# Optimization experiments

Hardware: AMD Instinct MI355X
Metric: run time of the kernel (lower is better)

Reference implementation:

```python
import jax, jax.numpy as jnp
import numpy as np

N, T, S, E, H, DFF = 4, 2048, 2048, 512, 8, 2048
DH = E // H
EPS = 1e-5


def layer_norm(x, w, b):
    m = jnp.mean(x, axis=-1, keepdims=True)
    v = jnp.mean(jnp.square(x - m), axis=-1, keepdims=True)
    return (x - m) * jax.lax.rsqrt(v + EPS) * w + b


def mha(q, k, v, wq, bq, wk, bk, wv, bv, wo, bo, mask=None):
    # q: (N,Tq,E), k/v: (N,Tk,E); torch Linear convention: y = x @ W.T + b
    Nq, Tq, _ = q.shape
    Tk = k.shape[1]
    Q = (q @ wq.T + bq).reshape(Nq, Tq, H, DH).transpose(0, 2, 1, 3)  # (N,H,Tq,DH)
    K = (k @ wk.T + bk).reshape(Nq, Tk, H, DH).transpose(0, 2, 1, 3)
    V = (v @ wv.T + bv).reshape(Nq, Tk, H, DH).transpose(0, 2, 1, 3)
    scores = jnp.einsum('bhtd,bhsd->bhts', Q, K) * (1.0 / np.sqrt(DH))  # (N,H,Tq,Tk)
    if mask is not None:
        scores = jnp.where(mask, scores, jnp.float32(-1e9))
    attn = jax.nn.softmax(scores, axis=-1)
    out = jnp.einsum('bhts,bhsd->bhtd', attn, V)  # (N,H,Tq,DH)
    out = out.transpose(0, 2, 1, 3).reshape(Nq, Tq, E)
    return out @ wo.T + bo


def setup_inputs() -> dict:
    key = jax.random.key(0)
    ks = jax.random.split(key, 20)
    s = 0.02

    def lin(k, out_d, in_d):
        return jax.random.normal(k, (out_d, in_d), jnp.float32) * s

    inp = {
        'tgt': jax.random.normal(ks[0], (N, T, E), jnp.float32),
        'memory': jax.random.normal(ks[1], (N, S, E), jnp.float32),
        'tgt_mask': jnp.tril(jnp.ones((T, T), dtype=bool)),  # causal (T,T)
        # self-attention params
        'sa_wq': lin(ks[2], E, E), 'sa_bq': jnp.zeros((E,), jnp.float32),
        'sa_wk': lin(ks[3], E, E), 'sa_bk': jnp.zeros((E,), jnp.float32),
        'sa_wv': lin(ks[4], E, E), 'sa_bv': jnp.zeros((E,), jnp.float32),
        'sa_wo': lin(ks[5], E, E), 'sa_bo': jnp.zeros((E,), jnp.float32),
        # cross-attention params
        'ca_wq': lin(ks[6], E, E), 'ca_bq': jnp.zeros((E,), jnp.float32),
        'ca_wk': lin(ks[7], E, E), 'ca_bk': jnp.zeros((E,), jnp.float32),
        'ca_wv': lin(ks[8], E, E), 'ca_bv': jnp.zeros((E,), jnp.float32),
        'ca_wo': lin(ks[9], E, E), 'ca_bo': jnp.zeros((E,), jnp.float32),
        # FFN params
        'w1': lin(ks[10], DFF, E), 'b1': jnp.zeros((DFF,), jnp.float32),
        'w2': lin(ks[11], E, DFF), 'b2': jnp.zeros((E,), jnp.float32),
        # LayerNorm params
        'ln1_w': jnp.ones((E,), jnp.float32), 'ln1_b': jnp.zeros((E,), jnp.float32),
        'ln2_w': jnp.ones((E,), jnp.float32), 'ln2_b': jnp.zeros((E,), jnp.float32),
        'ln3_w': jnp.ones((E,), jnp.float32), 'ln3_b': jnp.zeros((E,), jnp.float32),
    }
    return inp


def reference(tgt, memory, tgt_mask,
              sa_wq, sa_bq, sa_wk, sa_bk, sa_wv, sa_bv, sa_wo, sa_bo,
              ca_wq, ca_bq, ca_wk, ca_bk, ca_wv, ca_bv, ca_wo, ca_bo,
              w1, b1, w2, b2,
              ln1_w, ln1_b, ln2_w, ln2_b, ln3_w, ln3_b):
    # stage 1: masked self-attention + residual + LN (dropout=0 / eval mode)
    sa = mha(tgt, tgt, tgt, sa_wq, sa_bq, sa_wk, sa_bk, sa_wv, sa_bv, sa_wo, sa_bo, mask=tgt_mask)
    x = layer_norm(tgt + sa, ln1_w, ln1_b)
    # stage 2: cross-attention over encoder memory + residual + LN
    ca = mha(x, memory, memory, ca_wq, ca_bq, ca_wk, ca_bk, ca_wv, ca_bv, ca_wo, ca_bo)
    x = layer_norm(x + ca, ln2_w, ln2_b)
    # stage 3: FFN (ReLU) + residual + LN
    mlp = jax.nn.relu(x @ w1.T + b1) @ w2.T + b2
    out = layer_norm(x + mlp, ln3_w, ln3_b)
    return out
```

## Files before the change

### kernel.cpp

```cpp
#include <hip/hip_runtime.h>
#include <hip/hip_bf16.h>
#include <cstdint>

typedef short short8 __attribute__((ext_vector_type(8)));
typedef short short4v __attribute__((ext_vector_type(4)));
typedef float f32x4 __attribute__((ext_vector_type(4)));
typedef float f32x16 __attribute__((ext_vector_type(16)));

#define GLL16(gp, lp) __builtin_amdgcn_global_load_lds( \
    (const __attribute__((address_space(1))) unsigned int*)(gp), \
    (__attribute__((address_space(3))) unsigned int*)(lp), 16, 0, 0)

__device__ __forceinline__ float bf2f(ushort u) {
    union { unsigned int i; float f; } v; v.i = ((unsigned int)u) << 16; return v.f;
}
__device__ __forceinline__ ushort f2bf(float f) {
    union { float f; unsigned int u; } v; v.f = f;
    unsigned int r = v.u + 0x7FFFu + ((v.u >> 16) & 1u);
    return (ushort)(r >> 16);
}
__device__ __forceinline__ int cvtpk_bf16(float lo, float hi) {
    int r;
    asm("v_cvt_pk_bf16_f32 %0, %1, %2" : "=v"(r) : "v"(lo), "v"(hi));
    return r;
}
__device__ __forceinline__ void plane32_swap(int& a, int& b) {
    asm volatile("v_permlane32_swap_b32 %0, %1" : "+v"(a), "+v"(b));
}

struct CvtArgs {
    const float* src[12];
    ushort*      dst[12];
};
__global__ __launch_bounds__(256) void f2b_all(CvtArgs a)
{
    int id = blockIdx.x;
    int seg, boff;
    if (id < 4096)       { seg = 0; boff = id; }
    else if (id < 8192)  { seg = 1; boff = id - 4096; }
    else if (id < 10240) { int t = id - 8192; seg = 2 + (t >> 8); boff = t & 255; }
    else if (id < 11264) { seg = 10; boff = id - 10240; }
    else                 { seg = 11; boff = id - 11264; }
    int i = (boff * 256 + threadIdx.x) * 4;
    f32x4 v = *(const f32x4*)(a.src[seg] + i);
    short4v o;
#pragma unroll
    for (int e = 0; e < 4; ++e) o[e] = (short)f2bf(v[e]);
    *(short4v*)(a.dst[seg] + i) = o;
}

template<int MODE, int DEPTH>
__global__ __launch_bounds__(256) void gemm_bt(
    const ushort* __restrict__ A, const ushort* __restrict__ W,
    const float* __restrict__ b0, const float* __restrict__ b1,
    const float* __restrict__ b2,
    ushort* __restrict__ C0, ushort* __restrict__ C1, ushort* __restrict__ C2,
    int M, int N, int K)
{
    __shared__ ushort As[DEPTH][128 * 32];
    __shared__ ushort Bs[DEPTH][128 * 32];
    const int tid = threadIdx.x;
    const int l  = tid & 63;
    const int w  = tid >> 6;
    const int wr = w >> 1, wc = w & 1;
    const int bn = blockIdx.x, bm = blockIdx.y;
    const int lg = l >> 4, li = l & 15;

    const ushort* Ab = A + (size_t)(bm * 128) * K;
    const ushort* Bb = W + (size_t)(bn * 128) * K;

    f32x4 acc[4][4] = {};

    const int r0 = tid >> 2,         s0 = (tid & 3) ^ ((r0 >> 2) & 3);
    const int r1 = (tid + 256) >> 2, s1 = (tid & 3) ^ ((r1 >> 2) & 3);

    auto stage = [&](int buf, int kt) {
        const ushort* Ak = Ab + kt * 32;
        const ushort* Bk = Bb + kt * 32;
        GLL16(Ak + (size_t)r0 * K + s0 * 8, &As[buf][tid * 8]);
        GLL16(Ak + (size_t)r1 * K + s1 * 8, &As[buf][(tid + 256) * 8]);
        GLL16(Bk + (size_t)r0 * K + s0 * 8, &Bs[buf][tid * 8]);
        GLL16(Bk + (size_t)r1 * K + s1 * 8, &Bs[buf][(tid + 256) * 8]);
    };

    const int nk = K >> 5;
#pragma unroll
    for (int p = 0; p < DEPTH - 1; ++p)
        if (p < nk) stage(p, p);

    for (int kt = 0; kt < nk; ++kt) {
        const int b = kt & (DEPTH - 1);
        const int nxt = kt + DEPTH - 1;
        if (nxt < nk) stage(nxt & (DEPTH - 1), nxt);
        const int rem = nk - 1 - kt;
        const int fl = rem < DEPTH - 1 ? rem : DEPTH - 1;
        if (fl >= 3)      asm volatile("s_waitcnt vmcnt(12)" ::: "memory");
        else if (fl == 2) asm volatile("s_waitcnt vmcnt(8)"  ::: "memory");
        else if (fl == 1) asm volatile("s_waitcnt vmcnt(4)"  ::: "memory");
        else              asm volatile("s_waitcnt vmcnt(0)"  ::: "memory");
        __builtin_amdgcn_s_barrier();
        __builtin_amdgcn_sched_barrier(0);

        short8 af[4], bfr[4];
#pragma unroll
        for (int mi = 0; mi < 4; ++mi) {
            int row = wr * 64 + mi * 16 + li;
            int ch  = lg ^ ((row >> 2) & 3);
            af[mi] = *(const short8*)(&As[b][row * 32 + ch * 8]);
        }
#pragma unroll
        for (int ni = 0; ni < 4; ++ni) {
            int row = wc * 64 + ni * 16 + li;
            int ch  = lg ^ ((row >> 2) & 3);
            bfr[ni] = *(const short8*)(&Bs[b][row * 32 + ch * 8]);
        }
#pragma unroll
        for (int mi = 0; mi < 4; ++mi)
#pragma unroll
            for (int ni = 0; ni < 4; ++ni)
                acc[mi][ni] = __builtin_amdgcn_mfma_f32_16x16x32_bf16(
                    af[mi], bfr[ni], acc[mi][ni], 0, 0, 0);

        __builtin_amdgcn_sched_barrier(0);
        asm volatile("s_waitcnt lgkmcnt(0)" ::: "memory");
        __builtin_amdgcn_s_barrier();
    }

    const int crow0 = bm * 128 + wr * 64 + lg * 4;
    const int ccol0 = bn * 128 + wc * 64 + li;
    const int sec = (MODE == 2 || MODE == 3) ? (bn >> 2) : 0;
    const float* bp = b0;
    ushort* Cw = C0;
    bool vsec = false;
    if (MODE == 2) {
        bp = (sec == 0) ? b0 : (sec == 1) ? b1 : b2;
        Cw = (sec == 0) ? C0 : (sec == 1) ? C1 : C2;
        vsec = (sec == 2);
    } else if (MODE == 3) {
        bp = (sec == 0) ? b0 : b1;
        Cw = (sec == 0) ? C0 : C1;
        vsec = (sec == 1);
    }
    const int Nout = (MODE == 2 || MODE == 3) ? 512 : N;

#pragma unroll
    for (int ni = 0; ni < 4; ++ni) {
        int col = ccol0 + ni * 16;
        int cl  = (MODE == 2 || MODE == 3) ? (col & 511) : col;
        float bv = bp[cl];
#pragma unroll
        for (int mi = 0; mi < 4; ++mi) {
            int row = crow0 + mi * 16;
            if (vsec) {
                int n = row >> 11, t = row & 2047;
                int h = cl >> 6,  d = cl & 63;
                size_t base = ((size_t)((n * 8 + h) * 64 + d)) * 2048 + t;
                short4v pk;
#pragma unroll
                for (int r = 0; r < 4; ++r) pk[r] = (short)f2bf(acc[mi][ni][r] + bv);
                *(short4v*)(Cw + base) = pk;
            } else {
#pragma unroll
                for (int r = 0; r < 4; ++r) {
                    float v = acc[mi][ni][r] + bv;
                    if (MODE == 1) v = fmaxf(v, 0.f);
                    Cw[(size_t)(row + r) * Nout + cl] = f2bf(v);
                }
            }
        }
    }
}

template<bool CAUSAL>
__global__ __launch_bounds__(256) void attn_kernel(
    const ushort* __restrict__ Q, const ushort* __restrict__ K,
    const ushort* __restrict__ Vt, ushort* __restrict__ P0,
    ushort* __restrict__ P1, float* __restrict__ Ls, int Tk)
{
    __shared__ ushort SH[16384];
    const int tid = threadIdx.x;
    const int l = tid & 63, wq = tid >> 6;
    const int c = l & 31, hi = l >> 5;

    int qt, nh, ck;
    if (CAUSAL) {
        int g = (int)blockIdx.x >> 6;
        qt = (g < 8) ? (15 - g) : (g - 8);
        int r = blockIdx.x & 63;
        nh = r >> 1; ck = r & 1;
    } else {
        int pos = ((int)blockIdx.x & 7) * 128 + ((int)blockIdx.x >> 3);
        nh = pos >> 5; ck = (pos >> 4) & 1; qt = pos & 15;
    }
    const int q0 = qt * 128;
    const int n = nh >> 3, h = nh & 7;
    const int qrow = q0 + wq * 32 + c;

    short8 qf[4];
#pragma unroll
    for (int s = 0; s < 4; ++s)
        qf[s] = *(const short8*)(Q + (size_t)(n * 2048 + qrow) * 512
                                   + h * 64 + s * 16 + hi * 8);

    f32x16 oacc[2] = {};
    float lsum = 0.f;

    const ushort* Kbase = K + (size_t)(n * 2048) * 512 + h * 64;
    const ushort* Vbase = Vt + (size_t)nh * 64 * Tk;

    const int rowA = tid >> 3;
    const int csA  = (tid & 7) ^ (rowA & 7);

    auto stage = [&](int buf, int j0) {
        ushort* kd = SH + buf * 4096;
        ushort* vd = SH + 8192 + buf * 4096;
        GLL16(Kbase + (size_t)(j0 + rowA) * 512 + csA * 8,      kd + tid * 8);
        GLL16(Kbase + (size_t)(j0 + rowA + 32) * 512 + csA * 8, kd + (tid + 256) * 8);
        GLL16(Vbase + (size_t)rowA * Tk + j0 + csA * 8,         vd + tid * 8);
        GLL16(Vbase + (size_t)(rowA + 32) * Tk + j0 + csA * 8,  vd + (tid + 256) * 8);
    };

    const float SC = 0.125f * 1.44269504f;
    const int cnt = CAUSAL ? (qt + 1) : (Tk >> 7);

    stage(0, ck * 64);
    for (int s = 0; s < cnt; ++s) {
        const int b  = s & 1;
        const int j0 = (ck + 2 * s) << 6;
        if (s + 1 < cnt) {
            stage(b ^ 1, j0 + 128);
            asm volatile("s_waitcnt vmcnt(4)" ::: "memory");
        } else {
            asm volatile("s_waitcnt vmcnt(0)" ::: "memory");
        }
        __builtin_amdgcn_s_barrier();
        __builtin_amdgcn_sched_barrier(0);

        const ushort* kls = SH + b * 4096;
        const ushort* vls = SH + 8192 + b * 4096;

        f32x16 sacc[2] = {};
        __builtin_amdgcn_s_setprio(1);
#pragma unroll
        for (int ks = 0; ks < 4; ++ks) {
#pragma unroll
            for (int t2 = 0; t2 < 2; ++t2) {
                int row = t2 * 32 + c;
                int ch  = (ks * 2 + hi) ^ (row & 7);
                short8 kf = *(const short8*)(kls + row * 64 + ch * 8);
                sacc[t2] = __builtin_amdgcn_mfma_f32_32x32x16_bf16(
                    kf, qf[ks], sacc[t2], 0, 0, 0);
            }
        }
        __builtin_amdgcn_s_setprio(0);

        const bool domask = CAUSAL && (j0 + 64 > q0);
#pragma unroll
        for (int t2 = 0; t2 < 2; ++t2) {
            float pv[16];
#pragma unroll
            for (int reg = 0; reg < 16; ++reg) {
                float p = exp2f(sacc[t2][reg] * SC);
                if (domask) {
                    int jg = j0 + t2 * 32 + (reg & 3) + 8 * (reg >> 2) + 4 * hi;
                    if (jg > qrow) p = 0.f;
                }
                lsum += p;
                pv[reg] = p;
            }
            int X0 = cvtpk_bf16(pv[0],  pv[1]),  Y0 = cvtpk_bf16(pv[2],  pv[3]);
            int X1 = cvtpk_bf16(pv[4],  pv[5]),  Y1 = cvtpk_bf16(pv[6],  pv[7]);
            int X2 = cvtpk_bf16(pv[8],  pv[9]),  Y2 = cvtpk_bf16(pv[10], pv[11]);
            int X3 = cvtpk_bf16(pv[12], pv[13]), Y3 = cvtpk_bf16(pv[14], pv[15]);
            plane32_swap(X0, X1); plane32_swap(Y0, Y1);
            plane32_swap(X2, X3); plane32_swap(Y2, Y3);
            union { int i[4]; short8 s; } pa0 = {{X0, Y0, X1, Y1}},
                                          pa1 = {{X2, Y2, X3, Y3}};
            __builtin_amdgcn_s_setprio(1);
#pragma unroll
            for (int sp = 0; sp < 2; ++sp) {
                short8 pa = sp ? pa1.s : pa0.s;
#pragma unroll
                for (int dc = 0; dc < 2; ++dc) {
                    int row = dc * 32 + c;
                    int ch  = (t2 * 4 + sp * 2 + hi) ^ (row & 7);
                    short8 vb = *(const short8*)(vls + row * 64 + ch * 8);
                    oacc[dc] = __builtin_amdgcn_mfma_f32_32x32x16_bf16(
                        pa, vb, oacc[dc], 0, 0, 0);
                }
            }
            __builtin_amdgcn_s_setprio(0);
        }

        __builtin_amdgcn_sched_barrier(0);
        asm volatile("s_waitcnt lgkmcnt(0)" ::: "memory");
        __builtin_amdgcn_s_barrier();
    }

    lsum += __shfl_xor(lsum, 32);

    ushort* Pw = ck ? P1 : P0;
    if (hi == 0)
        Ls[ck * 65536 + nh * 2048 + q0 + wq * 32 + c] = lsum;
#pragma unroll
    for (int dc = 0; dc < 2; ++dc)
#pragma unroll
        for (int reg = 0; reg < 16; ++reg) {
            int qloc = (reg & 3) + 8 * (reg >> 2) + 4 * hi;
            size_t off = (size_t)(n * 2048 + q0 + wq * 32 + qloc) * 512
                       + h * 64 + dc * 32 + c;
            Pw[off] = f2bf(oacc[dc][reg]);
        }
}

__global__ __launch_bounds__(256) void attn_merge(
    const ushort* __restrict__ P0, const ushort* __restrict__ P1,
    const float* __restrict__ Ls, ushort* __restrict__ out)
{
    const int row = blockIdx.x * 4 + (threadIdx.x >> 6);
    const int l = threadIdx.x & 63;
    const size_t off = (size_t)row * 512 + l * 8;
    const int n = row >> 11, q = row & 2047, h = l >> 3;
    const int lidx = (n * 8 + h) * 2048 + q;
    float linv = 1.f / (Ls[lidx] + Ls[65536 + lidx]);
    short8 a = *(const short8*)(P0 + off);
    short8 b = *(const short8*)(P1 + off);
    short8 o;
#pragma unroll
    for (int e = 0; e < 8; ++e)
        o[e] = (short)f2bf((bf2f((ushort)a[e]) + bf2f((ushort)b[e])) * linv);
    *(short8*)(out + off) = o;
}

template<int F32OUT>
__global__ __launch_bounds__(256) void ln_kernel(
    const ushort* __restrict__ X, const ushort* __restrict__ Y,
    const float* __restrict__ W, const float* __restrict__ B,
    void* __restrict__ outp)
{
    const int row = blockIdx.x * 4 + (threadIdx.x >> 6);
    const int l = threadIdx.x & 63;
    const size_t off = (size_t)row * 512 + l * 8;
    short8 xv = *(const short8*)(X + off);
    short8 yv = *(const short8*)(Y + off);
    float v[8], s = 0.f, s2 = 0.f;
#pragma unroll
    for (int e = 0; e < 8; ++e) {
        float f = bf2f((ushort)xv[e]) + bf2f((ushort)yv[e]);
        v[e] = f; s += f; s2 += f * f;
    }
#pragma unroll
    for (int m = 1; m < 64; m <<= 1) {
        s  += __shfl_xor(s,  m);
        s2 += __shfl_xor(s2, m);
    }
    float mean = s * (1.f / 512.f);
    float var  = s2 * (1.f / 512.f) - mean * mean;
    float rs   = rsqrtf(var + 1e-5f);
    f32x4 w0 = *(const f32x4*)(W + l * 8);
    f32x4 w1 = *(const f32x4*)(W + l * 8 + 4);
    f32x4 b0 = *(const f32x4*)(B + l * 8);
    f32x4 b1 = *(const f32x4*)(B + l * 8 + 4);
    float wv[8] = {w0[0], w0[1], w0[2], w0[3], w1[0], w1[1], w1[2], w1[3]};
    float bv[8] = {b0[0], b0[1], b0[2], b0[3], b1[0], b1[1], b1[2], b1[3]};
    if (F32OUT) {
        float* out = (float*)outp;
#pragma unroll
        for (int e = 0; e < 8; ++e)
            out[off + e] = (v[e] - mean) * rs * wv[e] + bv[e];
    } else {
        ushort* out = (ushort*)outp;
        short8 ov;
#pragma unroll
        for (int e = 0; e < 8; ++e)
            ov[e] = (short)f2bf((v[e] - mean) * rs * wv[e] + bv[e]);
        *(short8*)(out + off) = ov;
    }
}

extern "C" void kernel_launch(void* const* d_in, const int* in_sizes, int n_in,
                              void* d_out, int out_size, void* d_ws, size_t ws_size,
                              hipStream_t stream)
{
    (void)in_sizes; (void)n_in; (void)out_size; (void)ws_size;
    const float* tgt  = (const float*)d_in[0];
    const float* mem  = (const float*)d_in[1];
    const float* sa_wq = (const float*)d_in[3];
    const float* sa_bq = (const float*)d_in[4];
    const float* sa_wk = (const float*)d_in[5];
    const float* sa_bk = (const float*)d_in[6];
    const float* sa_wv = (const float*)d_in[7];
    const float* sa_bv = (const float*)d_in[8];
    const float* sa_wo = (const float*)d_in[9];
    const float* sa_bo = (const float*)d_in[10];
    const float* ca_wq = (const float*)d_in[11];
    const float* ca_bq = (const float*)d_in[12];
    const float* ca_wk = (const float*)d_in[13];
    const float* ca_bk = (const float*)d_in[14];
    const float* ca_wv = (const float*)d_in[15];
    const float* ca_bv = (const float*)d_in[16];
    const float* ca_wo = (const float*)d_in[17];
    const float* ca_bo = (const float*)d_in[18];
    const float* w1    = (const float*)d_in[19];
    const float* b1    = (const float*)d_in[20];
    const float* w2    = (const float*)d_in[21];
    const float* b2    = (const float*)d_in[22];
    const float* ln1w  = (const float*)d_in[23];
    const float* ln1b  = (const float*)d_in[24];
    const float* ln2w  = (const float*)d_in[25];
    const float* ln2b  = (const float*)d_in[26];
    const float* ln3w  = (const float*)d_in[27];
    const float* ln3b  = (const float*)d_in[28];

    const size_t SE = (size_t)8192 * 512;
    const size_t EE = (size_t)512 * 512;
    ushort* ws = (ushort*)d_ws;
    ushort* Wb   = ws;
    ushort* bsqkv = Wb;
    ushort* bswo  = Wb + 3 * EE;
    ushort* bcwq  = Wb + 4 * EE;
    ushort* bckv  = Wb + 5 * EE;
    ushort* bcwo  = Wb + 7 * EE;
    ushort* bw1   = Wb + 8 * EE;
    ushort* bw2   = bw1 + 4 * EE;
    ushort* tgtb = Wb + 16 * EE;
    ushort* memb = tgtb + SE;
    ushort* Qb   = memb + SE;
    ushort* Kb   = Qb + SE;
    ushort* Vb   = Kb + SE;
    ushort* X1   = Vb + SE;
    ushort* AO   = X1 + SE;
    float*  LsBuf = (float*)(AO + SE);
    ushort* PO   = Qb;
    ushort* X2   = tgtb;
    ushort* Hb   = Qb;

    dim3 blk(256);
    dim3 gqkv(12, 64);
    dim3 gkv(8, 64);
    dim3 g512(4, 64);
    dim3 g2048(16, 64);
    dim3 ga(1024);
    dim3 gln(2048);

    CvtArgs ca;
    ca.src[0] = tgt;    ca.dst[0] = tgtb;
    ca.src[1] = mem;    ca.dst[1] = memb;
    ca.src[2] = sa_wq;  ca.dst[2] = bsqkv;
    ca.src[3] = sa_wk;  ca.dst[3] = bsqkv + EE;
    ca.src[4] = sa_wv;  ca.dst[4] = bsqkv + 2 * EE;
    ca.src[5] = sa_wo;  ca.dst[5] = bswo;
    ca.src[6] = ca_wq;  ca.dst[6] = bcwq;
    ca.src[7] = ca_wk;  ca.dst[7] = bckv;
    ca.src[8] = ca_wv;  ca.dst[8] = bckv + EE;
    ca.src[9] = ca_wo;  ca.dst[9] = bcwo;
    ca.src[10] = w1;    ca.dst[10] = bw1;
    ca.src[11] = w2;    ca.dst[11] = bw2;
    f2b_all<<<12288, blk, 0, stream>>>(ca);

    gemm_bt<2, 2><<<gqkv, blk, 0, stream>>>(tgtb, bsqkv, sa_bq, sa_bk, sa_bv,
                                            Qb, Kb, Vb, 8192, 1536, 512);
    attn_kernel<true><<<ga, blk, 0, stream>>>(Qb, Kb, Vb, AO, X1, LsBuf, 2048);
    attn_merge<<<gln, blk, 0, stream>>>(AO, X1, LsBuf, AO);
    gemm_bt<0, 4><<<g512, blk, 0, stream>>>(AO, bswo, sa_bo, nullptr, nullptr,
                                            PO, nullptr, nullptr, 8192, 512, 512);
    ln_kernel<0><<<gln, blk, 0, stream>>>(tgtb, PO, ln1w, ln1b, X1);

    gemm_bt<0, 4><<<g512, blk, 0, stream>>>(X1, bcwq, ca_bq, nullptr, nullptr,
                                            Qb, nullptr, nullptr, 8192, 512, 512);
    gemm_bt<3, 2><<<gkv, blk, 0, stream>>>(memb, bckv, ca_bk, ca_bv, nullptr,
                                           Kb, Vb, nullptr, 8192, 1024, 512);
    attn_kernel<false><<<ga, blk, 0, stream>>>(Qb, Kb, Vb, AO, tgtb, LsBuf, 2048);
    attn_merge<<<gln, blk, 0, stream>>>(AO, tgtb, LsBuf, AO);
    gemm_bt<0, 4><<<g512, blk, 0, stream>>>(AO, bcwo, ca_bo, nullptr, nullptr,
                                            PO, nullptr, nullptr, 8192, 512, 512);
    ln_kernel<0><<<gln, blk, 0, stream>>>(X1, PO, ln2w, ln2b, X2);

    gemm_bt<1, 2><<<g2048, blk, 0, stream>>>(X2, bw1, b1, nullptr, nullptr,
                                             Hb, nullptr, nullptr, 8192, 2048, 512);
    gemm_bt<0, 4><<<g512, blk, 0, stream>>>(Hb, bw2, b2, nullptr, nullptr,
                                            AO, nullptr, nullptr, 8192, 512, 2048);
    ln_kernel<1><<<gln, blk, 0, stream>>>(X2, AO, ln3w, ln3b, d_out);
}
```

Measured before the change: 308.4 us.

## Use 128x64 tiles for N=512 GEMMs, fold softmax scale into Q, MFMA row sums

Adds a TN template parameter so the N=512 GEMMs run with 128x64 tiles. That doubles their grid from 256 to 512 blocks, filling more CUs, and the vmcnt waits are adjusted for three loads per stage. The softmax scale (1/sqrt(64)·log2e) is moved into the Q projection epilogue, so attention can call raw v_exp_f32 on the scores. The per-lane scalar row sum is replaced by an MFMA against a vector of ones, which takes work off the VALU. The risks are more A-tile reloads and bf16 rounding of P in the denominator.

```diff
diff --git a/kernel.cpp b/kernel.cpp
--- a/kernel.cpp
+++ b/kernel.cpp
@@ -10,6 +10,7 @@
 #define GLL16(gp, lp) __builtin_amdgcn_global_load_lds( \
     (const __attribute__((address_space(1))) unsigned int*)(gp), \
     (__attribute__((address_space(3))) unsigned int*)(lp), 16, 0, 0)
+#define WAITV(n) asm volatile("s_waitcnt vmcnt(" #n ")" ::: "memory")
 
 __device__ __forceinline__ float bf2f(ushort u) {
     union { unsigned int i; float f; } v; v.i = ((unsigned int)u) << 16; return v.f;
@@ -27,6 +28,13 @@
 __device__ __forceinline__ void plane32_swap(int& a, int& b) {
     asm volatile("v_permlane32_swap_b32 %0, %1" : "+v"(a), "+v"(b));
 }
+__device__ __forceinline__ float fast_exp2(float x) {
+    float r;
+    asm("v_exp_f32 %0, %1" : "=v"(r) : "v"(x));
+    return r;
+}
+
+#define SCQ 0.18033688f
 
 struct CvtArgs {
     const float* src[12];
@@ -49,7 +57,7 @@
     *(short4v*)(a.dst[seg] + i) = o;
 }
 
-template<int MODE, int DEPTH>
+template<int MODE, int DEPTH, int TN>
 __global__ __launch_bounds__(256) void gemm_bt(
     const ushort* __restrict__ A, const ushort* __restrict__ W,
     const float* __restrict__ b0, const float* __restrict__ b1,
@@ -57,8 +65,10 @@
     ushort* __restrict__ C0, ushort* __restrict__ C1, ushort* __restrict__ C2,
     int M, int N, int K)
 {
+    constexpr int NI = TN / 32;
+    constexpr int L  = (TN == 128) ? 4 : 3;
     __shared__ ushort As[DEPTH][128 * 32];
-    __shared__ ushort Bs[DEPTH][128 * 32];
+    __shared__ ushort Bs[DEPTH][TN * 32];
     const int tid = threadIdx.x;
     const int l  = tid & 63;
     const int w  = tid >> 6;
@@ -67,9 +77,9 @@
     const int lg = l >> 4, li = l & 15;
 
     const ushort* Ab = A + (size_t)(bm * 128) * K;
-    const ushort* Bb = W + (size_t)(bn * 128) * K;
-
-    f32x4 acc[4][4] = {};
+    const ushort* Bb = W + (size_t)(bn * TN) * K;
+
+    f32x4 acc[4][NI] = {};
 
     const int r0 = tid >> 2,         s0 = (tid & 3) ^ ((r0 >> 2) & 3);
     const int r1 = (tid + 256) >> 2, s1 = (tid & 3) ^ ((r1 >> 2) & 3);
@@ -80,7 +90,8 @@
         GLL16(Ak + (size_t)r0 * K + s0 * 8, &As[buf][tid * 8]);
         GLL16(Ak + (size_t)r1 * K + s1 * 8, &As[buf][(tid + 256) * 8]);
         GLL16(Bk + (size_t)r0 * K + s0 * 8, &Bs[buf][tid * 8]);
-        GLL16(Bk + (size_t)r1 * K + s1 * 8, &Bs[buf][(tid + 256) * 8]);
+        if (TN == 128)
+            GLL16(Bk + (size_t)r1 * K + s1 * 8, &Bs[buf][(tid + 256) * 8]);
     };
 
     const int nk = K >> 5;
@@ -94,14 +105,21 @@
         if (nxt < nk) stage(nxt & (DEPTH - 1), nxt);
         const int rem = nk - 1 - kt;
         const int fl = rem < DEPTH - 1 ? rem : DEPTH - 1;
-        if (fl >= 3)      asm volatile("s_waitcnt vmcnt(12)" ::: "memory");
-        else if (fl == 2) asm volatile("s_waitcnt vmcnt(8)"  ::: "memory");
-        else if (fl == 1) asm volatile("s_waitcnt vmcnt(4)"  ::: "memory");
-        else              asm volatile("s_waitcnt vmcnt(0)"  ::: "memory");
+        if (L == 4) {
+            if (fl >= 3)      WAITV(12);
+            else if (fl == 2) WAITV(8);
+            else if (fl == 1) WAITV(4);
+            else              WAITV(0);
+        } else {
+            if (fl >= 3)      WAITV(9);
+            else if (fl == 2) WAITV(6);
+            else if (fl == 1) WAITV(3);
+            else              WAITV(0);
+        }
         __builtin_amdgcn_s_barrier();
         __builtin_amdgcn_sched_barrier(0);
 
-        short8 af[4], bfr[4];
+        short8 af[4], bfr[NI];
 #pragma unroll
         for (int mi = 0; mi < 4; ++mi) {
             int row = wr * 64 + mi * 16 + li;
@@ -109,15 +127,15 @@
             af[mi] = *(const short8*)(&As[b][row * 32 + ch * 8]);
         }
 #pragma unroll
-        for (int ni = 0; ni < 4; ++ni) {
-            int row = wc * 64 + ni * 16 + li;
+        for (int ni = 0; ni < NI; ++ni) {
+            int row = wc * (TN / 2) + ni * 16 + li;
             int ch  = lg ^ ((row >> 2) & 3);
             bfr[ni] = *(const short8*)(&Bs[b][row * 32 + ch * 8]);
         }
 #pragma unroll
         for (int mi = 0; mi < 4; ++mi)
 #pragma unroll
-            for (int ni = 0; ni < 4; ++ni)
+            for (int ni = 0; ni < NI; ++ni)
                 acc[mi][ni] = __builtin_amdgcn_mfma_f32_16x16x32_bf16(
                     af[mi], bfr[ni], acc[mi][ni], 0, 0, 0);
 
@@ -127,7 +145,7 @@
     }
 
     const int crow0 = bm * 128 + wr * 64 + lg * 4;
-    const int ccol0 = bn * 128 + wc * 64 + li;
+    const int ccol0 = bn * TN + wc * (TN / 2) + li;
     const int sec = (MODE == 2 || MODE == 3) ? (bn >> 2) : 0;
     const float* bp = b0;
     ushort* Cw = C0;
@@ -142,9 +160,10 @@
         vsec = (sec == 1);
     }
     const int Nout = (MODE == 2 || MODE == 3) ? 512 : N;
-
-#pragma unroll
-    for (int ni = 0; ni < 4; ++ni) {
+    const float scl = (MODE == 4 || (MODE == 2 && sec == 0)) ? SCQ : 1.f;
+
+#pragma unroll
+    for (int ni = 0; ni < NI; ++ni) {
         int col = ccol0 + ni * 16;
         int cl  = (MODE == 2 || MODE == 3) ? (col & 511) : col;
         float bv = bp[cl];
@@ -162,7 +181,7 @@
             } else {
 #pragma unroll
                 for (int r = 0; r < 4; ++r) {
-                    float v = acc[mi][ni][r] + bv;
+                    float v = (acc[mi][ni][r] + bv) * scl;
                     if (MODE == 1) v = fmaxf(v, 0.f);
                     Cw[(size_t)(row + r) * Nout + cl] = f2bf(v);
                 }
@@ -203,7 +222,9 @@
                                    + h * 64 + s * 16 + hi * 8);
 
     f32x16 oacc[2] = {};
-    float lsum = 0.f;
+    f32x16 oS = {};
+    const short ONE = (short)0x3F80;
+    const short8 ones = {ONE, ONE, ONE, ONE, ONE, ONE, ONE, ONE};
 
     const ushort* Kbase = K + (size_t)(n * 2048) * 512 + h * 64;
     const ushort* Vbase = Vt + (size_t)nh * 64 * Tk;
@@ -220,7 +241,6 @@
         GLL16(Vbase + (size_t)(rowA + 32) * Tk + j0 + csA * 8,  vd + (tid + 256) * 8);
     };
 
-    const float SC = 0.125f * 1.44269504f;
     const int cnt = CAUSAL ? (qt + 1) : (Tk >> 7);
 
     stage(0, ck * 64);
@@ -229,9 +249,9 @@
         const int j0 = (ck + 2 * s) << 6;
         if (s + 1 < cnt) {
             stage(b ^ 1, j0 + 128);
-            asm volatile("s_waitcnt vmcnt(4)" ::: "memory");
+            WAITV(4);
         } else {
-            asm volatile("s_waitcnt vmcnt(0)" ::: "memory");
+            WAITV(0);
         }
         __builtin_amdgcn_s_barrier();
         __builtin_amdgcn_sched_barrier(0);
@@ -260,12 +280,11 @@
             float pv[16];
 #pragma unroll
             for (int reg = 0; reg < 16; ++reg) {
-                float p = exp2f(sacc[t2][reg] * SC);
+                float p = fast_exp2(sacc[t2][reg]);
                 if (domask) {
                     int jg = j0 + t2 * 32 + (reg & 3) + 8 * (reg >> 2) + 4 * hi;
                     if (jg > qrow) p = 0.f;
                 }
-                lsum += p;
                 pv[reg] = p;
             }
             int X0 = cvtpk_bf16(pv[0],  pv[1]),  Y0 = cvtpk_bf16(pv[2],  pv[3]);
@@ -277,6 +296,8 @@
             union { int i[4]; short8 s; } pa0 = {{X0, Y0, X1, Y1}},
                                           pa1 = {{X2, Y2, X3, Y3}};
             __builtin_amdgcn_s_setprio(1);
+            oS = __builtin_amdgcn_mfma_f32_32x32x16_bf16(pa0.s, ones, oS, 0, 0, 0);
+            oS = __builtin_amdgcn_mfma_f32_32x32x16_bf16(pa1.s, ones, oS, 0, 0, 0);
 #pragma unroll
             for (int sp = 0; sp < 2; ++sp) {
                 short8 pa = sp ? pa1.s : pa0.s;
@@ -297,11 +318,14 @@
         __builtin_amdgcn_s_barrier();
     }
 
-    lsum += __shfl_xor(lsum, 32);
-
     ushort* Pw = ck ? P1 : P0;
-    if (hi == 0)
-        Ls[ck * 65536 + nh * 2048 + q0 + wq * 32 + c] = lsum;
+    if (c == 0) {
+#pragma unroll
+        for (int reg = 0; reg < 16; ++reg) {
+            int qloc = (reg & 3) + 8 * (reg >> 2) + 4 * hi;
+            Ls[ck * 65536 + nh * 2048 + q0 + wq * 32 + qloc] = oS[reg];
+        }
+    }
 #pragma unroll
     for (int dc = 0; dc < 2; ++dc)
 #pragma unroll
@@ -438,7 +462,7 @@
     dim3 blk(256);
     dim3 gqkv(12, 64);
     dim3 gkv(8, 64);
-    dim3 g512(4, 64);
+    dim3 g64n(8, 64);
     dim3 g2048(16, 64);
     dim3 ga(1024);
     dim3 gln(2048);
@@ -458,27 +482,27 @@
     ca.src[11] = w2;    ca.dst[11] = bw2;
     f2b_all<<<12288, blk, 0, stream>>>(ca);
 
-    gemm_bt<2, 2><<<gqkv, blk, 0, stream>>>(tgtb, bsqkv, sa_bq, sa_bk, sa_bv,
-                                            Qb, Kb, Vb, 8192, 1536, 512);
+    gemm_bt<2, 2, 128><<<gqkv, blk, 0, stream>>>(tgtb, bsqkv, sa_bq, sa_bk, sa_bv,
+                                                 Qb, Kb, Vb, 8192, 1536, 512);
     attn_kernel<true><<<ga, blk, 0, stream>>>(Qb, Kb, Vb, AO, X1, LsBuf, 2048);
     attn_merge<<<gln, blk, 0, stream>>>(AO, X1, LsBuf, AO);
-    gemm_bt<0, 4><<<g512, blk, 0, stream>>>(AO, bswo, sa_bo, nullptr, nullptr,
-                                            PO, nullptr, nullptr, 8192, 512, 512);
+    gemm_bt<0, 4, 64><<<g64n, blk, 0, stream>>>(AO, bswo, sa_bo, nullptr, nullptr,
+                                                PO, nullptr, nullptr, 8192, 512, 512);
     ln_kernel<0><<<gln, blk, 0, stream>>>(tgtb, PO, ln1w, ln1b, X1);
 
-    gemm_bt<0, 4><<<g512, blk, 0, stream>>>(X1, bcwq, ca_bq, nullptr, nullptr,
-                                            Qb, nullptr, nullptr, 8192, 512, 512);
-    gemm_bt<3, 2><<<gkv, blk, 0, stream>>>(memb, bckv, ca_bk, ca_bv, nullptr,
-                                           Kb, Vb, nullptr, 8192, 1024, 512);
+    gemm_bt<4, 4, 64><<<g64n, blk, 0, stream>>>(X1, bcwq, ca_bq, nullptr, nullptr,
+                                                Qb, nullptr, nullptr, 8192, 512, 512);
+    gemm_bt<3, 2, 128><<<gkv, blk, 0, stream>>>(memb, bckv, ca_bk, ca_bv, nullptr,
+                                                Kb, Vb, nullptr, 8192, 1024, 512);
     attn_kernel<false><<<ga, blk, 0, stream>>>(Qb, Kb, Vb, AO, tgtb, LsBuf, 2048);
     attn_merge<<<gln, blk, 0, stream>>>(AO, tgtb, LsBuf, AO);
-    gemm_bt<0, 4><<<g512, blk, 0, stream>>>(AO, bcwo, ca_bo, nullptr, nullptr,
-                                            PO, nullptr, nullptr, 8192, 512, 512);
+    gemm_bt<0, 4, 64><<<g64n, blk, 0, stream>>>(AO, bcwo, ca_bo, nullptr, nullptr,
+                                                PO, nullptr, nullptr, 8192, 512, 512);
     ln_kernel<0><<<gln, blk, 0, stream>>>(X1, PO, ln2w, ln2b, X2);
 
-    gemm_bt<1, 2><<<g2048, blk, 0, stream>>>(X2, bw1, b1, nullptr, nullptr,
-                                             Hb, nullptr, nullptr, 8192, 2048, 512);
-    gemm_bt<0, 4><<<g512, blk, 0, stream>>>(Hb, bw2, b2, nullptr, nullptr,
-                                            AO, nullptr, nullptr, 8192, 512, 2048);
+    gemm_bt<1, 2, 128><<<g2048, blk, 0, stream>>>(X2, bw1, b1, nullptr, nullptr,
+                                                  Hb, nullptr, nullptr, 8192, 2048, 512);
+    gemm_bt<0, 4, 64><<<g64n, blk, 0, stream>>>(Hb, bw2, b2, nullptr, nullptr,
+                                                AO, nullptr, nullptr, 8192, 512, 2048);
     ln_kernel<1><<<gln, blk, 0, stream>>>(X2, AO, ln3w, ln3b, d_out);
 }
```

After: 284.8 us (median of 2 runs). 7.6% less time.
